# Optimization experiments

Hardware: AMD Instinct MI355X
Metric: run time of the kernel (lower is better)

The kernel has to match this reference:

```python
import jax, jax.numpy as jnp
import numpy as np

LAGS = 2
LATENT = 8
EMB = 8
HID = 64
N_HIDDEN = 2  # num_layers - 1 hidden Linear layers inside each MLP
G_IN = HID + LAGS * LATENT + 1  # 81


def _leaky(h):
    return jnp.where(h >= 0, h, 0.1 * h)  # LeakyReLU(0.1)


def _mlp(x, W1, b1, Wh, bh, W2, b2):
    h = _leaky(x @ W1 + b1)
    for j in range(Wh.shape[0]):
        h = _leaky(h @ Wh[j] + bh[j])
    return h @ W2 + b2


def setup_inputs() -> dict:
    key = jax.random.key(0)
    ks = jax.random.split(key, 16)

    def lin(k, fan_in, shape):
        return jax.random.normal(k, shape, dtype=jnp.float32) / np.sqrt(fan_in)

    inp = {}
    inp["x"] = jax.random.normal(ks[0], (64, 2048, LATENT), dtype=jnp.float32)
    inp["embeddings"] = jax.random.normal(ks[1], (64, 2048, EMB), dtype=jnp.float32)
    # fc: MLP(EMB, HID, HID, depth=3)
    inp["fcW1"] = lin(ks[2], EMB, (EMB, HID))
    inp["fcb1"] = jnp.zeros((HID,), jnp.float32)
    inp["fcWh"] = lin(ks[3], HID, (N_HIDDEN, HID, HID))
    inp["fcbh"] = jnp.zeros((N_HIDDEN, HID), jnp.float32)
    inp["fcW2"] = lin(ks[4], HID, (HID, HID))
    inp["fcb2"] = jnp.zeros((HID,), jnp.float32)
    # gs: LATENT stacked MLP(G_IN, HID, 1, depth=3)
    inp["gW1"] = lin(ks[5], G_IN, (LATENT, G_IN, HID))
    inp["gb1"] = jnp.zeros((LATENT, HID), jnp.float32)
    inp["gWh"] = lin(ks[6], HID, (LATENT, N_HIDDEN, HID, HID))
    inp["gbh"] = jnp.zeros((LATENT, N_HIDDEN, HID), jnp.float32)
    inp["gW2"] = lin(ks[7], HID, (LATENT, HID, 1))
    inp["gb2"] = jnp.zeros((LATENT, 1), jnp.float32)
    return inp


def reference(x, embeddings, fcW1, fcb1, fcWh, fcbh, fcW2, fcb2,
              gW1, gb1, gWh, gbh, gW2, gb2):
    B, TL, D = x.shape
    length = TL - LAGS
    # unfold(1, lags+1, 1).transpose(2,3) -> [B, length, lags+1, D]
    batch_x = jnp.stack([x[:, t:t + length] for t in range(LAGS + 1)], axis=2)
    emb = _mlp(embeddings, fcW1, fcb1, fcWh, fcbh, fcW2, fcb2)  # [B, TL, HID]
    emb = emb[:, -length:].reshape(B * length, HID)
    bx = batch_x.reshape(B * length, LAGS + 1, D)
    x_lags = bx[:, :-1].reshape(B * length, LAGS * D)
    x_t = bx[:, -1]  # [N, D]
    base = jnp.concatenate([emb, x_lags], axis=-1)  # [N, HID+LAGS*D]
    N, base_dim = base.shape
    # per-dim inputs: [D, N, G_IN]; only last column differs across dims
    inputs = jnp.concatenate(
        [jnp.broadcast_to(base[None], (D, N, base_dim)), x_t.T[:, :, None]],
        axis=-1)

    def per_dim(inp, W1, b1, Wh, bh, W2, b2):
        f = lambda z: _mlp(z, W1, b1, Wh, bh, W2, b2)
        # jacfwd last column == JVP with e_last tangent
        tangent = jnp.zeros_like(inp).at[:, -1].set(1.0)
        out, dout = jax.jvp(f, (inp,), (tangent,))
        return out[:, 0], jnp.log(jnp.abs(dout[:, 0]))

    res, logd = jax.vmap(per_dim)(inputs, gW1, gb1, gWh, gbh, gW2, gb2)
    residuals = res.T.reshape(B, length, D)
    log_abs_det_jacobian = jnp.sum(logd, axis=0).reshape(B, length)
    return residuals, log_abs_det_jacobian
```

## Files before the change

### kernel.cpp

```cpp
#include <hip/hip_runtime.h>
#include <hip/hip_bf16.h>
#include <math.h>

#define BB   64
#define TT   2048
#define DD   8
#define HH   64
#define LLEN 2046
#define NN   (BB*LLEN)
#define GIN  81

#define NG   (NN/32)
#define WPB  8
#define ZSTR 36

__device__ __forceinline__ int zoff(int row, int sb) {
    return row * ZSTR + (((sb + (row >> 3)) & 7) << 2);
}

template<int K, bool ACT>
__device__ __forceinline__ void fwd_layer(float* zr,
                                          const float* __restrict__ W,
                                          const float* __restrict__ bias)
{
    float acc[HH];
#pragma unroll
    for (int j = 0; j < HH; ++j) acc[j] = bias[j];
    for (int k = 0; k < K; ++k) {
        const float zk = zr[k];
        const float* wr = W + k * HH;
#pragma unroll
        for (int j = 0; j < HH; ++j) acc[j] = fmaf(zk, wr[j], acc[j]);
    }
#pragma unroll
    for (int j = 0; j < HH; ++j) {
        float v = acc[j];
        if (ACT) v = (v >= 0.f) ? v : 0.1f * v;
        zr[j] = v;
    }
}

__global__ __launch_bounds__(192) void emb_mlp_kernel(
    const float* __restrict__ emb_in,
    const float* __restrict__ W1, const float* __restrict__ b1,
    const float* __restrict__ Wh, const float* __restrict__ bh,
    const float* __restrict__ W2, const float* __restrict__ b2,
    float* __restrict__ embT)
{
    __shared__ float zrow[192][65];
    const int tid = threadIdx.x;
    const int n = blockIdx.x * 192 + tid;
    const int b = n / LLEN;
    const int l = n - b * LLEN;
    float* zr = zrow[tid];

    const float* ep = emb_in + ((size_t)(b * TT + (l + 2))) * 8;
    {
        float4 e0 = *(const float4*)ep;
        float4 e1 = *(const float4*)(ep + 4);
        zr[0] = e0.x; zr[1] = e0.y; zr[2] = e0.z; zr[3] = e0.w;
        zr[4] = e1.x; zr[5] = e1.y; zr[6] = e1.z; zr[7] = e1.w;
    }

    fwd_layer<8,  true >(zr, W1, b1);
    fwd_layer<HH, true >(zr, Wh,            bh);
    fwd_layer<HH, true >(zr, Wh + HH * HH,  bh + HH);
    fwd_layer<HH, false>(zr, W2, b2);

    float* op = embT + ((size_t)(n >> 5)) * 2048 + (n & 31);
#pragma unroll
    for (int j = 0; j < HH; ++j) op[j * 32] = zr[j];
}

__global__ __launch_bounds__(WPB * 64, 1) void gmlp_kernel(
    const float* __restrict__ x,
    const float* __restrict__ embT,
    const float* __restrict__ gW1, const float* __restrict__ gb1,
    const float* __restrict__ gWh, const float* __restrict__ gbh,
    const float* __restrict__ gW2, const float* __restrict__ gb2,
    float* __restrict__ resid, float* __restrict__ logd)
{
    __shared__ __align__(16) float zb[WPB][128 * ZSTR];

    const int tid  = threadIdx.x;
    const int lane = tid & 63;
    const int w    = tid >> 6;
    const int d    = blockIdx.y;
    const int gid  = blockIdx.x * WPB + w;
    if (gid >= NG) return;

    float* Z = zb[w];
    const int sg = lane >> 3;
    const int jg = lane & 7;
    const int n0 = gid * 32;

    const float* eb = embT + (size_t)gid * 2048;
#pragma unroll
    for (int i = 0; i < 8; ++i) {
        float4 v = *(const float4*)&eb[i * 256 + lane * 4];
        const int row = i * 8 + (lane >> 3);
        *(float4*)&Z[zoff(row, lane & 7)] = v;
    }
    {
        const int s = lane & 31, h = lane >> 5;
        const int n = n0 + s;
        const int b = n / LLEN, l = n - b * LLEN;
        const float* xp = x + ((size_t)(b * TT + l)) * DD;
        float4 xv0 = *(const float4*)(xp + h * 8);
        float4 xv1 = *(const float4*)(xp + h * 8 + 4);
        float xv[8] = { xv0.x, xv0.y, xv0.z, xv0.w, xv1.x, xv1.y, xv1.z, xv1.w };
#pragma unroll
        for (int r = 0; r < 8; ++r) {
            const int R = 64 + h * 8 + r;
            Z[zoff(R, s >> 2) + (s & 3)] = xv[r];
        }
        if (h == 0) {
            const float xt = xp[16 + d];
            Z[zoff(80, s >> 2) + (s & 3)] = xt;
        }
    }

    const float* W1 = gW1 + (size_t)d * GIN * HH + jg * 8;
    const float4 b1a = *(const float4*)&gb1[d * HH + jg * 8];
    const float4 b1b = *(const float4*)&gb1[d * HH + jg * 8 + 4];

    float f[4][8];
#pragma unroll
    for (int si = 0; si < 4; ++si) {
        f[si][0] = b1a.x; f[si][1] = b1a.y; f[si][2] = b1a.z; f[si][3] = b1a.w;
        f[si][4] = b1b.x; f[si][5] = b1b.y; f[si][6] = b1b.z; f[si][7] = b1b.w;
    }

    __builtin_amdgcn_s_setprio(1);
#pragma unroll 8
    for (int k = 0; k < GIN; ++k) {
        const float4 wa = *(const float4*)&W1[(size_t)k * HH];
        const float4 wb = *(const float4*)&W1[(size_t)k * HH + 4];
        const float4 zq = *(const float4*)&Z[zoff(k, sg)];
        const float zs[4] = { zq.x, zq.y, zq.z, zq.w };
#pragma unroll
        for (int si = 0; si < 4; ++si) {
            f[si][0] = fmaf(zs[si], wa.x, f[si][0]);
            f[si][1] = fmaf(zs[si], wa.y, f[si][1]);
            f[si][2] = fmaf(zs[si], wa.z, f[si][2]);
            f[si][3] = fmaf(zs[si], wa.w, f[si][3]);
            f[si][4] = fmaf(zs[si], wb.x, f[si][4]);
            f[si][5] = fmaf(zs[si], wb.y, f[si][5]);
            f[si][6] = fmaf(zs[si], wb.z, f[si][6]);
            f[si][7] = fmaf(zs[si], wb.w, f[si][7]);
        }
    }
    __builtin_amdgcn_s_setprio(0);

    {
        const float4 w80a = *(const float4*)&W1[80 * HH];
        const float4 w80b = *(const float4*)&W1[80 * HH + 4];
        const float w80[8] = { w80a.x, w80a.y, w80a.z, w80a.w,
                               w80b.x, w80b.y, w80b.z, w80b.w };
        float zv[4][8], dv[4][8];
#pragma unroll
        for (int si = 0; si < 4; ++si)
#pragma unroll
            for (int jj = 0; jj < 8; ++jj) {
                const float m = (f[si][jj] >= 0.f) ? 1.f : 0.1f;
                zv[si][jj] = f[si][jj] * m;
                dv[si][jj] = w80[jj] * m;
            }
#pragma unroll
        for (int jj = 0; jj < 8; ++jj) {
            const int row = jg * 8 + jj;
            float4 q = { zv[0][jj], zv[1][jj], zv[2][jj], zv[3][jj] };
            *(float4*)&Z[zoff(row, sg)] = q;
            float4 p = { dv[0][jj], dv[1][jj], dv[2][jj], dv[3][jj] };
            *(float4*)&Z[zoff(64 + row, sg)] = p;
        }
    }

    const float* Whg = gWh + (size_t)d * 2 * HH * HH;
    float ff[4][8], dd[4][8];
#pragma unroll
    for (int hl = 0; hl < 2; ++hl) {
        const float* Wl = Whg + hl * (HH * HH) + jg * 8;
        const float4 ba = *(const float4*)&gbh[(d * 2 + hl) * HH + jg * 8];
        const float4 bb = *(const float4*)&gbh[(d * 2 + hl) * HH + jg * 8 + 4];
#pragma unroll
        for (int si = 0; si < 4; ++si) {
            ff[si][0] = ba.x; ff[si][1] = ba.y; ff[si][2] = ba.z; ff[si][3] = ba.w;
            ff[si][4] = bb.x; ff[si][5] = bb.y; ff[si][6] = bb.z; ff[si][7] = bb.w;
#pragma unroll
            for (int jj = 0; jj < 8; ++jj) dd[si][jj] = 0.f;
        }
        __builtin_amdgcn_s_setprio(1);
#pragma unroll 8
        for (int k = 0; k < HH; ++k) {
            const float4 wa = *(const float4*)&Wl[k * HH];
            const float4 wb = *(const float4*)&Wl[k * HH + 4];
            const float4 zq = *(const float4*)&Z[zoff(k, sg)];
            const float4 dq = *(const float4*)&Z[zoff(64 + k, sg)];
            const float zs[4] = { zq.x, zq.y, zq.z, zq.w };
            const float ds[4] = { dq.x, dq.y, dq.z, dq.w };
#pragma unroll
            for (int si = 0; si < 4; ++si) {
                ff[si][0] = fmaf(zs[si], wa.x, ff[si][0]);  dd[si][0] = fmaf(ds[si], wa.x, dd[si][0]);
                ff[si][1] = fmaf(zs[si], wa.y, ff[si][1]);  dd[si][1] = fmaf(ds[si], wa.y, dd[si][1]);
                ff[si][2] = fmaf(zs[si], wa.z, ff[si][2]);  dd[si][2] = fmaf(ds[si], wa.z, dd[si][2]);
                ff[si][3] = fmaf(zs[si], wa.w, ff[si][3]);  dd[si][3] = fmaf(ds[si], wa.w, dd[si][3]);
                ff[si][4] = fmaf(zs[si], wb.x, ff[si][4]);  dd[si][4] = fmaf(ds[si], wb.x, dd[si][4]);
                ff[si][5] = fmaf(zs[si], wb.y, ff[si][5]);  dd[si][5] = fmaf(ds[si], wb.y, dd[si][5]);
                ff[si][6] = fmaf(zs[si], wb.z, ff[si][6]);  dd[si][6] = fmaf(ds[si], wb.z, dd[si][6]);
                ff[si][7] = fmaf(zs[si], wb.w, ff[si][7]);  dd[si][7] = fmaf(ds[si], wb.w, dd[si][7]);
            }
        }
        __builtin_amdgcn_s_setprio(0);
#pragma unroll
        for (int si = 0; si < 4; ++si)
#pragma unroll
            for (int jj = 0; jj < 8; ++jj) {
                const float m = (ff[si][jj] >= 0.f) ? 1.f : 0.1f;
                ff[si][jj] *= m;
                dd[si][jj] *= m;
            }
        if (hl == 0) {
#pragma unroll
            for (int jj = 0; jj < 8; ++jj) {
                const int row = jg * 8 + jj;
                float4 q = { ff[0][jj], ff[1][jj], ff[2][jj], ff[3][jj] };
                *(float4*)&Z[zoff(row, sg)] = q;
                float4 p = { dd[0][jj], dd[1][jj], dd[2][jj], dd[3][jj] };
                *(float4*)&Z[zoff(64 + row, sg)] = p;
            }
        }
    }

    {
        const float4 w2a = *(const float4*)&gW2[d * HH + jg * 8];
        const float4 w2b = *(const float4*)&gW2[d * HH + jg * 8 + 4];
        const float b2 = gb2[d];
        float o[4], q[4];
#pragma unroll
        for (int si = 0; si < 4; ++si) {
            o[si] = ff[si][0]*w2a.x + ff[si][1]*w2a.y + ff[si][2]*w2a.z + ff[si][3]*w2a.w
                  + ff[si][4]*w2b.x + ff[si][5]*w2b.y + ff[si][6]*w2b.z + ff[si][7]*w2b.w;
            q[si] = dd[si][0]*w2a.x + dd[si][1]*w2a.y + dd[si][2]*w2a.z + dd[si][3]*w2a.w
                  + dd[si][4]*w2b.x + dd[si][5]*w2b.y + dd[si][6]*w2b.z + dd[si][7]*w2b.w;
#pragma unroll
            for (int m = 1; m <= 4; m <<= 1) {
                o[si] += __shfl_xor(o[si], m);
                q[si] += __shfl_xor(q[si], m);
            }
        }
        if (jg == 0) {
            const int nb = n0 + sg * 4;
            float4 lq;
            lq.x = __logf(fabsf(q[0])); lq.y = __logf(fabsf(q[1]));
            lq.z = __logf(fabsf(q[2])); lq.w = __logf(fabsf(q[3]));
#pragma unroll
            for (int si = 0; si < 4; ++si)
                resid[(size_t)(nb + si) * DD + d] = o[si] + b2;
            *(float4*)&logd[(size_t)d * NN + nb] = lq;
        }
    }
}

__global__ __launch_bounds__(256) void reduce_kernel(
    const float* __restrict__ logd, float* __restrict__ out)
{
    const int n = blockIdx.x * 256 + threadIdx.x;
    if (n >= NN) return;
    float s = 0.f;
#pragma unroll
    for (int d = 0; d < DD; ++d) s += logd[(size_t)d * NN + n];
    out[n] = s;
}

extern "C" void kernel_launch(void* const* d_in, const int* in_sizes, int n_in,
                              void* d_out, int out_size, void* d_ws, size_t ws_size,
                              hipStream_t stream)
{
    const float* x          = (const float*)d_in[0];
    const float* embeddings = (const float*)d_in[1];
    const float* fcW1 = (const float*)d_in[2];
    const float* fcb1 = (const float*)d_in[3];
    const float* fcWh = (const float*)d_in[4];
    const float* fcbh = (const float*)d_in[5];
    const float* fcW2 = (const float*)d_in[6];
    const float* fcb2 = (const float*)d_in[7];
    const float* gW1  = (const float*)d_in[8];
    const float* gb1  = (const float*)d_in[9];
    const float* gWh  = (const float*)d_in[10];
    const float* gbh  = (const float*)d_in[11];
    const float* gW2  = (const float*)d_in[12];
    const float* gb2  = (const float*)d_in[13];

    float* out  = (float*)d_out;
    float* embT = (float*)d_ws;
    float* logd = embT + (size_t)NN * HH;

    emb_mlp_kernel<<<dim3(NN / 192), 192, 0, stream>>>(
        embeddings, fcW1, fcb1, fcWh, fcbh, fcW2, fcb2, embT);

    gmlp_kernel<<<dim3((NG + WPB - 1) / WPB, DD), WPB * 64, 0, stream>>>(
        x, embT, gW1, gb1, gWh, gbh, gW2, gb2, out, logd);

    reduce_kernel<<<dim3((NN + 255) / 256), 256, 0, stream>>>(
        logd, out + (size_t)NN * DD);
}
```

Baseline: 677.9 us.

## Process multiple row groups per wave with register prefetch of next group's inputs

Each wave now loops over four consecutive 32-row groups instead of one. It issues the global loads for the next group's embeddings and lagged x values before the current group's hidden layers run, so load latency overlaps compute. Per-dimension biases and output weights are loaded once per wave and kept for all groups. The grid shrinks by a factor of four, which cuts available parallelism and raises register pressure from the prefetch buffers.

```diff
diff --git a/kernel.cpp b/kernel.cpp
--- a/kernel.cpp
+++ b/kernel.cpp
@@ -12,6 +12,7 @@
 
 #define NG   (NN/32)
 #define WPB  8
+#define GPW  4
 #define ZSTR 36
 
 __device__ __forceinline__ int zoff(int row, int sb) {
@@ -86,178 +87,197 @@
     const int lane = tid & 63;
     const int w    = tid >> 6;
     const int d    = blockIdx.y;
-    const int gid  = blockIdx.x * WPB + w;
-    if (gid >= NG) return;
+    const int g0   = (blockIdx.x * WPB + w) * GPW;
 
     float* Z = zb[w];
     const int sg = lane >> 3;
     const int jg = lane & 7;
-    const int n0 = gid * 32;
-
-    const float* eb = embT + (size_t)gid * 2048;
-#pragma unroll
-    for (int i = 0; i < 8; ++i) {
-        float4 v = *(const float4*)&eb[i * 256 + lane * 4];
-        const int row = i * 8 + (lane >> 3);
-        *(float4*)&Z[zoff(row, lane & 7)] = v;
-    }
-    {
-        const int s = lane & 31, h = lane >> 5;
-        const int n = n0 + s;
+
+    const float* W1 = gW1 + (size_t)d * GIN * HH + jg * 8;
+    const float* Whg = gWh + (size_t)d * 2 * HH * HH;
+    const float4 b1a = *(const float4*)&gb1[d * HH + jg * 8];
+    const float4 b1b = *(const float4*)&gb1[d * HH + jg * 8 + 4];
+    const float4 bh0a = *(const float4*)&gbh[(d * 2 + 0) * HH + jg * 8];
+    const float4 bh0b = *(const float4*)&gbh[(d * 2 + 0) * HH + jg * 8 + 4];
+    const float4 bh1a = *(const float4*)&gbh[(d * 2 + 1) * HH + jg * 8];
+    const float4 bh1b = *(const float4*)&gbh[(d * 2 + 1) * HH + jg * 8 + 4];
+    const float4 w2a = *(const float4*)&gW2[d * HH + jg * 8];
+    const float4 w2b = *(const float4*)&gW2[d * HH + jg * 8 + 4];
+    const float b2 = gb2[d];
+
+    float4 pe[8];
+    float  pxv[8], pxt;
+    const int s_ = lane & 31, h_ = lane >> 5;
+
+    auto issue_loads = [&](int gid) {
+        const float* eb = embT + (size_t)gid * 2048;
+#pragma unroll
+        for (int i = 0; i < 8; ++i)
+            pe[i] = *(const float4*)&eb[i * 256 + lane * 4];
+        const int n = gid * 32 + s_;
         const int b = n / LLEN, l = n - b * LLEN;
         const float* xp = x + ((size_t)(b * TT + l)) * DD;
-        float4 xv0 = *(const float4*)(xp + h * 8);
-        float4 xv1 = *(const float4*)(xp + h * 8 + 4);
-        float xv[8] = { xv0.x, xv0.y, xv0.z, xv0.w, xv1.x, xv1.y, xv1.z, xv1.w };
+        float4 xv0 = *(const float4*)(xp + h_ * 8);
+        float4 xv1 = *(const float4*)(xp + h_ * 8 + 4);
+        pxv[0] = xv0.x; pxv[1] = xv0.y; pxv[2] = xv0.z; pxv[3] = xv0.w;
+        pxv[4] = xv1.x; pxv[5] = xv1.y; pxv[6] = xv1.z; pxv[7] = xv1.w;
+        pxt = xp[16 + d];
+    };
+    auto write_zin = [&]() {
+#pragma unroll
+        for (int i = 0; i < 8; ++i) {
+            const int row = i * 8 + (lane >> 3);
+            *(float4*)&Z[zoff(row, lane & 7)] = pe[i];
+        }
 #pragma unroll
         for (int r = 0; r < 8; ++r) {
-            const int R = 64 + h * 8 + r;
-            Z[zoff(R, s >> 2) + (s & 3)] = xv[r];
-        }
-        if (h == 0) {
-            const float xt = xp[16 + d];
-            Z[zoff(80, s >> 2) + (s & 3)] = xt;
-        }
-    }
-
-    const float* W1 = gW1 + (size_t)d * GIN * HH + jg * 8;
-    const float4 b1a = *(const float4*)&gb1[d * HH + jg * 8];
-    const float4 b1b = *(const float4*)&gb1[d * HH + jg * 8 + 4];
-
-    float f[4][8];
-#pragma unroll
-    for (int si = 0; si < 4; ++si) {
-        f[si][0] = b1a.x; f[si][1] = b1a.y; f[si][2] = b1a.z; f[si][3] = b1a.w;
-        f[si][4] = b1b.x; f[si][5] = b1b.y; f[si][6] = b1b.z; f[si][7] = b1b.w;
-    }
-
-    __builtin_amdgcn_s_setprio(1);
-#pragma unroll 8
-    for (int k = 0; k < GIN; ++k) {
-        const float4 wa = *(const float4*)&W1[(size_t)k * HH];
-        const float4 wb = *(const float4*)&W1[(size_t)k * HH + 4];
-        const float4 zq = *(const float4*)&Z[zoff(k, sg)];
-        const float zs[4] = { zq.x, zq.y, zq.z, zq.w };
+            const int R = 64 + h_ * 8 + r;
+            Z[zoff(R, s_ >> 2) + (s_ & 3)] = pxv[r];
+        }
+        if (h_ == 0) Z[zoff(80, s_ >> 2) + (s_ & 3)] = pxt;
+    };
+
+    if (g0 < NG) issue_loads(g0);
+
+    for (int g = 0; g < GPW; ++g) {
+        const int gid = g0 + g;
+        if (gid >= NG) break;
+        const int n0 = gid * 32;
+
+        write_zin();
+
+        float f[4][8];
 #pragma unroll
         for (int si = 0; si < 4; ++si) {
-            f[si][0] = fmaf(zs[si], wa.x, f[si][0]);
-            f[si][1] = fmaf(zs[si], wa.y, f[si][1]);
-            f[si][2] = fmaf(zs[si], wa.z, f[si][2]);
-            f[si][3] = fmaf(zs[si], wa.w, f[si][3]);
-            f[si][4] = fmaf(zs[si], wb.x, f[si][4]);
-            f[si][5] = fmaf(zs[si], wb.y, f[si][5]);
-            f[si][6] = fmaf(zs[si], wb.z, f[si][6]);
-            f[si][7] = fmaf(zs[si], wb.w, f[si][7]);
-        }
-    }
-    __builtin_amdgcn_s_setprio(0);
-
-    {
-        const float4 w80a = *(const float4*)&W1[80 * HH];
-        const float4 w80b = *(const float4*)&W1[80 * HH + 4];
-        const float w80[8] = { w80a.x, w80a.y, w80a.z, w80a.w,
-                               w80b.x, w80b.y, w80b.z, w80b.w };
-        float zv[4][8], dv[4][8];
-#pragma unroll
-        for (int si = 0; si < 4; ++si)
-#pragma unroll
-            for (int jj = 0; jj < 8; ++jj) {
-                const float m = (f[si][jj] >= 0.f) ? 1.f : 0.1f;
-                zv[si][jj] = f[si][jj] * m;
-                dv[si][jj] = w80[jj] * m;
-            }
-#pragma unroll
-        for (int jj = 0; jj < 8; ++jj) {
-            const int row = jg * 8 + jj;
-            float4 q = { zv[0][jj], zv[1][jj], zv[2][jj], zv[3][jj] };
-            *(float4*)&Z[zoff(row, sg)] = q;
-            float4 p = { dv[0][jj], dv[1][jj], dv[2][jj], dv[3][jj] };
-            *(float4*)&Z[zoff(64 + row, sg)] = p;
-        }
-    }
-
-    const float* Whg = gWh + (size_t)d * 2 * HH * HH;
-    float ff[4][8], dd[4][8];
-#pragma unroll
-    for (int hl = 0; hl < 2; ++hl) {
-        const float* Wl = Whg + hl * (HH * HH) + jg * 8;
-        const float4 ba = *(const float4*)&gbh[(d * 2 + hl) * HH + jg * 8];
-        const float4 bb = *(const float4*)&gbh[(d * 2 + hl) * HH + jg * 8 + 4];
-#pragma unroll
-        for (int si = 0; si < 4; ++si) {
-            ff[si][0] = ba.x; ff[si][1] = ba.y; ff[si][2] = ba.z; ff[si][3] = ba.w;
-            ff[si][4] = bb.x; ff[si][5] = bb.y; ff[si][6] = bb.z; ff[si][7] = bb.w;
-#pragma unroll
-            for (int jj = 0; jj < 8; ++jj) dd[si][jj] = 0.f;
+            f[si][0] = b1a.x; f[si][1] = b1a.y; f[si][2] = b1a.z; f[si][3] = b1a.w;
+            f[si][4] = b1b.x; f[si][5] = b1b.y; f[si][6] = b1b.z; f[si][7] = b1b.w;
         }
         __builtin_amdgcn_s_setprio(1);
 #pragma unroll 8
-        for (int k = 0; k < HH; ++k) {
-            const float4 wa = *(const float4*)&Wl[k * HH];
-            const float4 wb = *(const float4*)&Wl[k * HH + 4];
+        for (int k = 0; k < GIN; ++k) {
+            const float4 wa = *(const float4*)&W1[(size_t)k * HH];
+            const float4 wb = *(const float4*)&W1[(size_t)k * HH + 4];
             const float4 zq = *(const float4*)&Z[zoff(k, sg)];
-            const float4 dq = *(const float4*)&Z[zoff(64 + k, sg)];
             const float zs[4] = { zq.x, zq.y, zq.z, zq.w };
-            const float ds[4] = { dq.x, dq.y, dq.z, dq.w };
 #pragma unroll
             for (int si = 0; si < 4; ++si) {
-                ff[si][0] = fmaf(zs[si], wa.x, ff[si][0]);  dd[si][0] = fmaf(ds[si], wa.x, dd[si][0]);
-                ff[si][1] = fmaf(zs[si], wa.y, ff[si][1]);  dd[si][1] = fmaf(ds[si], wa.y, dd[si][1]);
-                ff[si][2] = fmaf(zs[si], wa.z, ff[si][2]);  dd[si][2] = fmaf(ds[si], wa.z, dd[si][2]);
-                ff[si][3] = fmaf(zs[si], wa.w, ff[si][3]);  dd[si][3] = fmaf(ds[si], wa.w, dd[si][3]);
-                ff[si][4] = fmaf(zs[si], wb.x, ff[si][4]);  dd[si][4] = fmaf(ds[si], wb.x, dd[si][4]);
-                ff[si][5] = fmaf(zs[si], wb.y, ff[si][5]);  dd[si][5] = fmaf(ds[si], wb.y, dd[si][5]);
-                ff[si][6] = fmaf(zs[si], wb.z, ff[si][6]);  dd[si][6] = fmaf(ds[si], wb.z, dd[si][6]);
-                ff[si][7] = fmaf(zs[si], wb.w, ff[si][7]);  dd[si][7] = fmaf(ds[si], wb.w, dd[si][7]);
+                f[si][0] = fmaf(zs[si], wa.x, f[si][0]);
+                f[si][1] = fmaf(zs[si], wa.y, f[si][1]);
+                f[si][2] = fmaf(zs[si], wa.z, f[si][2]);
+                f[si][3] = fmaf(zs[si], wa.w, f[si][3]);
+                f[si][4] = fmaf(zs[si], wb.x, f[si][4]);
+                f[si][5] = fmaf(zs[si], wb.y, f[si][5]);
+                f[si][6] = fmaf(zs[si], wb.z, f[si][6]);
+                f[si][7] = fmaf(zs[si], wb.w, f[si][7]);
             }
         }
         __builtin_amdgcn_s_setprio(0);
-#pragma unroll
-        for (int si = 0; si < 4; ++si)
-#pragma unroll
-            for (int jj = 0; jj < 8; ++jj) {
-                const float m = (ff[si][jj] >= 0.f) ? 1.f : 0.1f;
-                ff[si][jj] *= m;
-                dd[si][jj] *= m;
-            }
-        if (hl == 0) {
+
+        {
+            const float4 w80a = *(const float4*)&W1[80 * HH];
+            const float4 w80b = *(const float4*)&W1[80 * HH + 4];
+            const float w80[8] = { w80a.x, w80a.y, w80a.z, w80a.w,
+                                   w80b.x, w80b.y, w80b.z, w80b.w };
+            float zv[4][8], dv[4][8];
+#pragma unroll
+            for (int si = 0; si < 4; ++si)
+#pragma unroll
+                for (int jj = 0; jj < 8; ++jj) {
+                    const float m = (f[si][jj] >= 0.f) ? 1.f : 0.1f;
+                    zv[si][jj] = f[si][jj] * m;
+                    dv[si][jj] = w80[jj] * m;
+                }
 #pragma unroll
             for (int jj = 0; jj < 8; ++jj) {
                 const int row = jg * 8 + jj;
-                float4 q = { ff[0][jj], ff[1][jj], ff[2][jj], ff[3][jj] };
+                float4 q = { zv[0][jj], zv[1][jj], zv[2][jj], zv[3][jj] };
                 *(float4*)&Z[zoff(row, sg)] = q;
-                float4 p = { dd[0][jj], dd[1][jj], dd[2][jj], dd[3][jj] };
+                float4 p = { dv[0][jj], dv[1][jj], dv[2][jj], dv[3][jj] };
                 *(float4*)&Z[zoff(64 + row, sg)] = p;
             }
         }
-    }
-
-    {
-        const float4 w2a = *(const float4*)&gW2[d * HH + jg * 8];
-        const float4 w2b = *(const float4*)&gW2[d * HH + jg * 8 + 4];
-        const float b2 = gb2[d];
-        float o[4], q[4];
-#pragma unroll
-        for (int si = 0; si < 4; ++si) {
-            o[si] = ff[si][0]*w2a.x + ff[si][1]*w2a.y + ff[si][2]*w2a.z + ff[si][3]*w2a.w
-                  + ff[si][4]*w2b.x + ff[si][5]*w2b.y + ff[si][6]*w2b.z + ff[si][7]*w2b.w;
-            q[si] = dd[si][0]*w2a.x + dd[si][1]*w2a.y + dd[si][2]*w2a.z + dd[si][3]*w2a.w
-                  + dd[si][4]*w2b.x + dd[si][5]*w2b.y + dd[si][6]*w2b.z + dd[si][7]*w2b.w;
-#pragma unroll
-            for (int m = 1; m <= 4; m <<= 1) {
-                o[si] += __shfl_xor(o[si], m);
-                q[si] += __shfl_xor(q[si], m);
-            }
-        }
-        if (jg == 0) {
-            const int nb = n0 + sg * 4;
-            float4 lq;
-            lq.x = __logf(fabsf(q[0])); lq.y = __logf(fabsf(q[1]));
-            lq.z = __logf(fabsf(q[2])); lq.w = __logf(fabsf(q[3]));
+
+        if (g + 1 < GPW && gid + 1 < NG) issue_loads(gid + 1);
+
+        float ff[4][8], dd[4][8];
+#pragma unroll
+        for (int hl = 0; hl < 2; ++hl) {
+            const float* Wl = Whg + hl * (HH * HH) + jg * 8;
+            const float4 ba = hl ? bh1a : bh0a;
+            const float4 bb = hl ? bh1b : bh0b;
+#pragma unroll
+            for (int si = 0; si < 4; ++si) {
+                ff[si][0] = ba.x; ff[si][1] = ba.y; ff[si][2] = ba.z; ff[si][3] = ba.w;
+                ff[si][4] = bb.x; ff[si][5] = bb.y; ff[si][6] = bb.z; ff[si][7] = bb.w;
+#pragma unroll
+                for (int jj = 0; jj < 8; ++jj) dd[si][jj] = 0.f;
+            }
+            __builtin_amdgcn_s_setprio(1);
+#pragma unroll 8
+            for (int k = 0; k < HH; ++k) {
+                const float4 wa = *(const float4*)&Wl[k * HH];
+                const float4 wb = *(const float4*)&Wl[k * HH + 4];
+                const float4 zq = *(const float4*)&Z[zoff(k, sg)];
+                const float4 dq = *(const float4*)&Z[zoff(64 + k, sg)];
+                const float zs[4] = { zq.x, zq.y, zq.z, zq.w };
+                const float ds[4] = { dq.x, dq.y, dq.z, dq.w };
+#pragma unroll
+                for (int si = 0; si < 4; ++si) {
+                    ff[si][0] = fmaf(zs[si], wa.x, ff[si][0]);  dd[si][0] = fmaf(ds[si], wa.x, dd[si][0]);
+                    ff[si][1] = fmaf(zs[si], wa.y, ff[si][1]);  dd[si][1] = fmaf(ds[si], wa.y, dd[si][1]);
+                    ff[si][2] = fmaf(zs[si], wa.z, ff[si][2]);  dd[si][2] = fmaf(ds[si], wa.z, dd[si][2]);
+                    ff[si][3] = fmaf(zs[si], wa.w, ff[si][3]);  dd[si][3] = fmaf(ds[si], wa.w, dd[si][3]);
+                    ff[si][4] = fmaf(zs[si], wb.x, ff[si][4]);  dd[si][4] = fmaf(ds[si], wb.x, dd[si][4]);
+                    ff[si][5] = fmaf(zs[si], wb.y, ff[si][5]);  dd[si][5] = fmaf(ds[si], wb.y, dd[si][5]);
+                    ff[si][6] = fmaf(zs[si], wb.z, ff[si][6]);  dd[si][6] = fmaf(ds[si], wb.z, dd[si][6]);
+                    ff[si][7] = fmaf(zs[si], wb.w, ff[si][7]);  dd[si][7] = fmaf(ds[si], wb.w, dd[si][7]);
+                }
+            }
+            __builtin_amdgcn_s_setprio(0);
 #pragma unroll
             for (int si = 0; si < 4; ++si)
-                resid[(size_t)(nb + si) * DD + d] = o[si] + b2;
-            *(float4*)&logd[(size_t)d * NN + nb] = lq;
+#pragma unroll
+                for (int jj = 0; jj < 8; ++jj) {
+                    const float m = (ff[si][jj] >= 0.f) ? 1.f : 0.1f;
+                    ff[si][jj] *= m;
+                    dd[si][jj] *= m;
+                }
+            if (hl == 0) {
+#pragma unroll
+                for (int jj = 0; jj < 8; ++jj) {
+                    const int row = jg * 8 + jj;
+                    float4 q = { ff[0][jj], ff[1][jj], ff[2][jj], ff[3][jj] };
+                    *(float4*)&Z[zoff(row, sg)] = q;
+                    float4 p = { dd[0][jj], dd[1][jj], dd[2][jj], dd[3][jj] };
+                    *(float4*)&Z[zoff(64 + row, sg)] = p;
+                }
+            }
+        }
+
+        {
+            float o[4], q[4];
+#pragma unroll
+            for (int si = 0; si < 4; ++si) {
+                o[si] = ff[si][0]*w2a.x + ff[si][1]*w2a.y + ff[si][2]*w2a.z + ff[si][3]*w2a.w
+                      + ff[si][4]*w2b.x + ff[si][5]*w2b.y + ff[si][6]*w2b.z + ff[si][7]*w2b.w;
+                q[si] = dd[si][0]*w2a.x + dd[si][1]*w2a.y + dd[si][2]*w2a.z + dd[si][3]*w2a.w
+                      + dd[si][4]*w2b.x + dd[si][5]*w2b.y + dd[si][6]*w2b.z + dd[si][7]*w2b.w;
+#pragma unroll
+                for (int m = 1; m <= 4; m <<= 1) {
+                    o[si] += __shfl_xor(o[si], m);
+                    q[si] += __shfl_xor(q[si], m);
+                }
+            }
+            if (jg == 0) {
+                const int nb = n0 + sg * 4;
+                float4 lq;
+                lq.x = __logf(fabsf(q[0])); lq.y = __logf(fabsf(q[1]));
+                lq.z = __logf(fabsf(q[2])); lq.w = __logf(fabsf(q[3]));
+#pragma unroll
+                for (int si = 0; si < 4; ++si)
+                    resid[(size_t)(nb + si) * DD + d] = o[si] + b2;
+                *(float4*)&logd[(size_t)d * NN + nb] = lq;
+            }
         }
     }
 }
@@ -299,7 +319,7 @@
     emb_mlp_kernel<<<dim3(NN / 192), 192, 0, stream>>>(
         embeddings, fcW1, fcb1, fcWh, fcbh, fcW2, fcb2, embT);
 
-    gmlp_kernel<<<dim3((NG + WPB - 1) / WPB, DD), WPB * 64, 0, stream>>>(
+    gmlp_kernel<<<dim3((NG + WPB * GPW - 1) / (WPB * GPW), DD), WPB * 64, 0, stream>>>(
         x, embT, gW1, gb1, gWh, gbh, gW2, gb2, out, logd);
 
     reduce_kernel<<<dim3((NN + 255) / 256), 256, 0, stream>>>(
```

Result: slower. 792.2 us (+16.9%).
